# Kernel optimization log

Measured on AMD Instinct MI355X. Metric: run time of the kernel, lower is better.

## Reference

```python
import jax, jax.numpy as jnp
import numpy as np

STRIDE, PAD, DIL = 1, 1, 1
EPS = 1e-12
RHO_LIM = 1.0 - 1e-6
PI = jnp.pi


def clamp_pg(x, lo=0.0):
    # clamp value but pass gradient through (clamp_preserve_grad)
    return x + jax.lax.stop_gradient(jnp.maximum(x, lo) - x)


def setup_inputs() -> dict:
    key = jax.random.key(0)
    B, N, T, K = 8, 128, 1024, 3
    k = jax.random.uniform(key, (B, B, N, T, 2), dtype=jnp.float32)
    leak = jnp.array(1.0, dtype=jnp.float32)
    alpha = jnp.full((1, 1, K), 1.0 / K, dtype=jnp.float32)
    beta = jnp.array(0.0, dtype=jnp.float32)
    return {"k": k, "leak": leak, "alpha": alpha, "beta": beta}


def reference(k, leak, alpha, beta):
    k_gp, k_ntk = k[..., 0], k[..., 1]          # (B,B,N,T) each
    B, _, N, T = k_gp.shape

    # v[b,t] = k_gp[b,b,0,t]  (diagonal over batch dims, first lag)
    ar = jnp.arange(B)
    v = k_gp[ar, ar, 0, :]                      # (B,T)
    v_pad = jnp.pad(v, ((0, 0), (0, N - 1)))    # (B, T+N-1)

    v_xx = v[:, None, None, :]                  # (B,1,1,T)
    idx = jnp.arange(N)[:, None] + jnp.arange(T)[None, :]  # (N,T)
    v_yy = v_pad[:, idx][None]                  # (1,B,N,T): v_pad[b, n+t]

    # calculate_statistics
    std_x = jnp.sqrt(jnp.maximum(v_xx, 0.0))
    std_y = jnp.sqrt(jnp.maximum(v_yy, 0.0))
    denom = jnp.maximum(std_x * std_y, EPS)
    rho = jnp.clip(k_gp / denom, -RHO_LIM, RHO_LIM)  # (B,B,N,T)

    a = clamp_pg(leak)
    theta = jnp.arccos(rho)
    s = jnp.sqrt(1.0 - rho * rho)
    one_m = (1.0 - a) ** 2
    coef = 1.0 + a * a
    # leaky-ReLU arccos kernel and its derivative kernel
    c0 = std_x * std_y / (2.0 * PI) * (one_m * s + rho * (coef * PI - one_m * theta))
    c1 = (coef * PI - one_m * theta) / (2.0 * PI)

    w = clamp_pg(alpha)                         # (1,1,K)

    def conv(x):  # x: (B,B,N,T) -> (B,B,N,T')
        y = jax.lax.conv_general_dilated(
            x.reshape(-1, 1, T), w, window_strides=(STRIDE,),
            padding=[(PAD, PAD)], rhs_dilation=(DIL,),
            dimension_numbers=("NCH", "OIH", "NCH"))
        return y.reshape(B, B, N, -1)

    kg = conv(c0)
    kn = conv(c1 * k_ntk) + kg

    b = clamp_pg(beta)
    kg = kg + b
    kn = kn + b
    return jnp.stack([kg, kn], axis=-1)
```

## Files before the change

### kernel.cpp

```cpp
#include <hip/hip_runtime.h>
#include <math.h>

#define BDIM 8
#define NDIM 128
#define TDIM 1024
#define TPB 512
#define ROWS 4
#define LSTRIDE 1028

#define EPS_F 1e-12f
#define RHO_LIM_F (1.0f - 1e-6f)
#define PI_F 3.14159265358979323846f


__device__ __forceinline__ void kfun(float kgp, float kntk, float vx, float vy,
                                     float one_m, float coef, bool fast,
                                     float& c0, float& cn)
{
    const float inv2pi = 0.15915494309189535f;
    const float p = sqrtf(fmaxf(vx, 0.0f) * fmaxf(vy, 0.0f));
    if (fast) {
        const float hc = 0.5f * coef;
        const float pr = p * RHO_LIM_F;
        c0 = hc * fminf(fmaxf(kgp, -pr), pr);
        cn = hc * kntk;
    } else {
        const float r  = fminf(fmaxf(kgp * __builtin_amdgcn_rcpf(fmaxf(p, EPS_F)), -RHO_LIM_F), RHO_LIM_F);
        const float th = acosf(r);
        const float s  = sqrtf(1.0f - r * r);
        const float br = coef * PI_F - one_m * th;
        c0 = p * inv2pi * (one_m * s + r * br);
        cn = br * inv2pi * kntk;
    }
}

__global__ __launch_bounds__(TPB) void conv_arccos_kernel(
    const float* __restrict__ k,
    const float* __restrict__ leak,
    const float* __restrict__ alpha,
    const float* __restrict__ beta,
    float* __restrict__ out)
{
    __shared__ float sc0[ROWS * LSTRIDE];
    __shared__ float scn[ROWS * LSTRIDE];

    const int base = blockIdx.x * ROWS;
    const int n0   = base % NDIM;
    const int bb   = base / NDIM;
    const int b2   = bb % BDIM;
    const int b1   = bb / BDIM;
    const int tid  = threadIdx.x;
    const int t    = tid * 2;

    const float a   = fmaxf(leak[0], 0.0f);
    const float w0  = fmaxf(alpha[0], 0.0f);
    const float w1  = fmaxf(alpha[1], 0.0f);
    const float w2  = fmaxf(alpha[2], 0.0f);
    const float bia = fmaxf(beta[0], 0.0f);

    const float one_m = (1.0f - a) * (1.0f - a);
    const float coef  = 1.0f + a * a;
    const bool  fast  = (one_m == 0.0f);

    const float2* vrx = (const float2*)(k) + (size_t)(b1 * BDIM + b1) * NDIM * TDIM;
    const float2* vry = (const float2*)(k) + (size_t)(b2 * BDIM + b2) * NDIM * TDIM;

    if (tid < ROWS * 2) {
        const int r   = tid >> 1;
        const int idx = r * LSTRIDE + ((tid & 1) ? (TDIM + 1) : 0);
        sc0[idx] = 0.0f;
        scn[idx] = 0.0f;
    }

    const float4 vx2 = ((const float4*)vrx)[tid];
    const float4* vyp = (const float4*)(vry + (n0 + t));
    const float4 vyA = vyp[0];
    const float4 vyB = vyp[1];
    float y0 = vyA.x, y1 = vyA.z, y2 = vyB.x, y3 = vyB.z;
    float y4 = vry[n0 + t + 4].x;
    const int ty = n0 + t;
    if (ty     >= TDIM) y0 = 0.0f;
    if (ty + 1 >= TDIM) y1 = 0.0f;
    if (ty + 2 >= TDIM) y2 = 0.0f;
    if (ty + 3 >= TDIM) y3 = 0.0f;
    if (ty + 4 >= TDIM) y4 = 0.0f;
    const float yv[6] = { y0, y1, y2, y3, y4, 0.0f };

    #pragma unroll
    for (int rl = 0; rl < ROWS; ++rl) {
        const float4 kv = ((const float4*)(k + (size_t)(base + rl) * TDIM * 2))[tid];
        float c00, cn0, c01, cn1;
        kfun(kv.x, kv.y, vx2.x, yv[rl],     one_m, coef, fast, c00, cn0);
        kfun(kv.z, kv.w, vx2.z, yv[rl + 1], one_m, coef, fast, c01, cn1);
        const int bi = rl * LSTRIDE + t + 1;
        sc0[bi]     = c00;
        sc0[bi + 1] = c01;
        scn[bi]     = cn0;
        scn[bi + 1] = cn1;
    }

    __syncthreads();

    #pragma unroll
    for (int rl = 0; rl < ROWS; ++rl) {
        const int bi = rl * LSTRIDE + t;
        const float c0l = sc0[bi], c00 = sc0[bi + 1], c01 = sc0[bi + 2], c0r = sc0[bi + 3];
        const float cnl = scn[bi], cn0 = scn[bi + 1], cn1 = scn[bi + 2], cnr = scn[bi + 3];

        const float kg0 = fmaf(w0, c0l, fmaf(w1, c00, fmaf(w2, c01, bia)));
        const float kg1 = fmaf(w0, c00, fmaf(w1, c01, fmaf(w2, c0r, bia)));
        const float kn0 = fmaf(w0, cnl, fmaf(w1, cn0, fmaf(w2, cn1, kg0)));
        const float kn1 = fmaf(w0, cn0, fmaf(w1, cn1, fmaf(w2, cnr, kg1)));

        float4 o;
        o.x = kg0; o.y = kn0; o.z = kg1; o.w = kn1;
        ((float4*)(out + (size_t)(base + rl) * TDIM * 2))[tid] = o;
    }
}

extern "C" void kernel_launch(void* const* d_in, const int* in_sizes, int n_in,
                              void* d_out, int out_size, void* d_ws, size_t ws_size,
                              hipStream_t stream) {
    const float* k     = (const float*)d_in[0];
    const float* leak  = (const float*)d_in[1];
    const float* alpha = (const float*)d_in[2];
    const float* beta  = (const float*)d_in[3];
    float* out = (float*)d_out;

    const int n_blocks = BDIM * BDIM * NDIM / ROWS;
    conv_arccos_kernel<<<n_blocks, TPB, 0, stream>>>(k, leak, alpha, beta, out);
}
```

Before: 118.5 us.

## Map one wavefront per row and exchange conv halos via shuffles

```diff
diff --git a/kernel.cpp b/kernel.cpp
--- a/kernel.cpp
+++ b/kernel.cpp
@@ -5,20 +5,20 @@
 #define NDIM 128
 #define TDIM 1024
 #define TPB 512
-#define ROWS 4
-#define LSTRIDE 1028
+#define ROWS_PER_BLOCK 8
 
 #define EPS_F 1e-12f
 #define RHO_LIM_F (1.0f - 1e-6f)
 #define PI_F 3.14159265358979323846f
 
+typedef float nfloat4 __attribute__((ext_vector_type(4)));
 
-__device__ __forceinline__ void kfun(float kgp, float kntk, float vx, float vy,
-                                     float one_m, float coef, bool fast,
-                                     float& c0, float& cn)
+__device__ __forceinline__ void kfun2(float kgp, float kntk, float sx, float sy,
+                                      float one_m, float coef, bool fast,
+                                      float& c0, float& cn)
 {
     const float inv2pi = 0.15915494309189535f;
-    const float p = sqrtf(fmaxf(vx, 0.0f) * fmaxf(vy, 0.0f));
+    const float p = sx * sy;
     if (fast) {
         const float hc = 0.5f * coef;
         const float pr = p * RHO_LIM_F;
@@ -41,16 +41,13 @@
     const float* __restrict__ beta,
     float* __restrict__ out)
 {
-    __shared__ float sc0[ROWS * LSTRIDE];
-    __shared__ float scn[ROWS * LSTRIDE];
-
-    const int base = blockIdx.x * ROWS;
-    const int n0   = base % NDIM;
-    const int bb   = base / NDIM;
-    const int b2   = bb % BDIM;
-    const int b1   = bb / BDIM;
-    const int tid  = threadIdx.x;
-    const int t    = tid * 2;
+    const int wid  = threadIdx.x >> 6;
+    const int lane = threadIdx.x & 63;
+    const int row  = blockIdx.x * ROWS_PER_BLOCK + wid;
+    const int n    = row & (NDIM - 1);
+    const int bb   = row >> 7;
+    const int b2   = bb & (BDIM - 1);
+    const int b1   = bb >> 3;
 
     const float a   = fmaxf(leak[0], 0.0f);
     const float w0  = fmaxf(alpha[0], 0.0f);
@@ -62,59 +59,59 @@
     const float coef  = 1.0f + a * a;
     const bool  fast  = (one_m == 0.0f);
 
-    const float2* vrx = (const float2*)(k) + (size_t)(b1 * BDIM + b1) * NDIM * TDIM;
-    const float2* vry = (const float2*)(k) + (size_t)(b2 * BDIM + b2) * NDIM * TDIM;
+    const nfloat4* krow = (const nfloat4*)(k + (size_t)row * TDIM * 2);
+    nfloat4*       orow = (nfloat4*)(out + (size_t)row * TDIM * 2);
+    const float2* vrx = (const float2*)k + (size_t)(b1 * BDIM + b1) * NDIM * TDIM;
+    const float2* vry = (const float2*)k + (size_t)(b2 * BDIM + b2) * NDIM * TDIM;
 
-    if (tid < ROWS * 2) {
-        const int r   = tid >> 1;
-        const int idx = r * LSTRIDE + ((tid & 1) ? (TDIM + 1) : 0);
-        sc0[idx] = 0.0f;
-        scn[idx] = 0.0f;
-    }
+    auto compute = [&](int m, float& c00, float& c01, float& cn0, float& cn1) {
+        const int p  = (m << 6) + lane;
+        const int t0 = p * 2;
+        const nfloat4 kv = __builtin_nontemporal_load(&krow[p]);
+        const float4 vx4 = *(const float4*)(vrx + t0);
+        const int e = n + t0;
+        const float2 vya = vry[e];
+        const float2 vyb = vry[e + 1];
+        const float y0 = (e     < TDIM) ? vya.x : 0.0f;
+        const float y1 = (e + 1 < TDIM) ? vyb.x : 0.0f;
+        const float sx0 = sqrtf(fmaxf(vx4.x, 0.0f));
+        const float sx1 = sqrtf(fmaxf(vx4.z, 0.0f));
+        const float sy0 = sqrtf(fmaxf(y0, 0.0f));
+        const float sy1 = sqrtf(fmaxf(y1, 0.0f));
+        kfun2(kv.x, kv.y, sx0, sy0, one_m, coef, fast, c00, cn0);
+        kfun2(kv.z, kv.w, sx1, sy1, one_m, coef, fast, c01, cn1);
+    };
 
-    const float4 vx2 = ((const float4*)vrx)[tid];
-    const float4* vyp = (const float4*)(vry + (n0 + t));
-    const float4 vyA = vyp[0];
-    const float4 vyB = vyp[1];
-    float y0 = vyA.x, y1 = vyA.z, y2 = vyB.x, y3 = vyB.z;
-    float y4 = vry[n0 + t + 4].x;
-    const int ty = n0 + t;
-    if (ty     >= TDIM) y0 = 0.0f;
-    if (ty + 1 >= TDIM) y1 = 0.0f;
-    if (ty + 2 >= TDIM) y2 = 0.0f;
-    if (ty + 3 >= TDIM) y3 = 0.0f;
-    if (ty + 4 >= TDIM) y4 = 0.0f;
-    const float yv[6] = { y0, y1, y2, y3, y4, 0.0f };
+    float c00, c01, cn0, cn1;
+    compute(0, c00, c01, cn0, cn1);
+    float pe0 = 0.0f, pen = 0.0f;
 
     #pragma unroll
-    for (int rl = 0; rl < ROWS; ++rl) {
-        const float4 kv = ((const float4*)(k + (size_t)(base + rl) * TDIM * 2))[tid];
-        float c00, cn0, c01, cn1;
-        kfun(kv.x, kv.y, vx2.x, yv[rl],     one_m, coef, fast, c00, cn0);
-        kfun(kv.z, kv.w, vx2.z, yv[rl + 1], one_m, coef, fast, c01, cn1);
-        const int bi = rl * LSTRIDE + t + 1;
-        sc0[bi]     = c00;
-        sc0[bi + 1] = c01;
-        scn[bi]     = cn0;
-        scn[bi + 1] = cn1;
-    }
+    for (int m = 0; m < 8; ++m) {
+        float n00 = 0.0f, n01 = 0.0f, nn0 = 0.0f, nn1 = 0.0f;
+        if (m < 7) compute(m + 1, n00, n01, nn0, nn1);
+        const float nx0 = __shfl(n00, 0);
+        const float nxn = __shfl(nn0, 0);
 
-    __syncthreads();
-
-    #pragma unroll
-    for (int rl = 0; rl < ROWS; ++rl) {
-        const int bi = rl * LSTRIDE + t;
-        const float c0l = sc0[bi], c00 = sc0[bi + 1], c01 = sc0[bi + 2], c0r = sc0[bi + 3];
-        const float cnl = scn[bi], cn0 = scn[bi + 1], cn1 = scn[bi + 2], cnr = scn[bi + 3];
+        float c0l = __shfl_up(c01, 1);
+        float cnl = __shfl_up(cn1, 1);
+        if (lane == 0) { c0l = pe0; cnl = pen; }
+        float c0r = __shfl_down(c00, 1);
+        float cnr = __shfl_down(cn0, 1);
+        if (lane == 63) { c0r = nx0; cnr = nxn; }
 
         const float kg0 = fmaf(w0, c0l, fmaf(w1, c00, fmaf(w2, c01, bia)));
         const float kg1 = fmaf(w0, c00, fmaf(w1, c01, fmaf(w2, c0r, bia)));
         const float kn0 = fmaf(w0, cnl, fmaf(w1, cn0, fmaf(w2, cn1, kg0)));
         const float kn1 = fmaf(w0, cn0, fmaf(w1, cn1, fmaf(w2, cnr, kg1)));
 
-        float4 o;
+        nfloat4 o;
         o.x = kg0; o.y = kn0; o.z = kg1; o.w = kn1;
-        ((float4*)(out + (size_t)(base + rl) * TDIM * 2))[tid] = o;
+        __builtin_nontemporal_store(o, &orow[(m << 6) + lane]);
+
+        pe0 = __shfl(c01, 63);
+        pen = __shfl(cn1, 63);
+        c00 = n00; c01 = n01; cn0 = nn0; cn1 = nn1;
     }
 }
 
@@ -127,6 +124,6 @@
     const float* beta  = (const float*)d_in[3];
     float* out = (float*)d_out;
 
-    const int n_blocks = BDIM * BDIM * NDIM / ROWS;
+    const int n_blocks = BDIM * BDIM * NDIM / ROWS_PER_BLOCK;
     conv_arccos_kernel<<<n_blocks, TPB, 0, stream>>>(k, leak, alpha, beta, out);
 }
```

New measurement: 129.9 us. 1.1x slower.

## Replace shared-memory halo exchange with redundant neighbor loads and recompute

Applied to the files above, without the earlier changes.

```diff
diff --git a/kernel.cpp b/kernel.cpp
--- a/kernel.cpp
+++ b/kernel.cpp
@@ -6,19 +6,17 @@
 #define TDIM 1024
 #define TPB 512
 #define ROWS 4
-#define LSTRIDE 1028
 
 #define EPS_F 1e-12f
 #define RHO_LIM_F (1.0f - 1e-6f)
 #define PI_F 3.14159265358979323846f
 
-
-__device__ __forceinline__ void kfun(float kgp, float kntk, float vx, float vy,
+__device__ __forceinline__ void kfun(float kgp, float kntk, float sx, float sy,
                                      float one_m, float coef, bool fast,
                                      float& c0, float& cn)
 {
     const float inv2pi = 0.15915494309189535f;
-    const float p = sqrtf(fmaxf(vx, 0.0f) * fmaxf(vy, 0.0f));
+    const float p = sx * sy;
     if (fast) {
         const float hc = 0.5f * coef;
         const float pr = p * RHO_LIM_F;
@@ -41,9 +39,6 @@
     const float* __restrict__ beta,
     float* __restrict__ out)
 {
-    __shared__ float sc0[ROWS * LSTRIDE];
-    __shared__ float scn[ROWS * LSTRIDE];
-
     const int base = blockIdx.x * ROWS;
     const int n0   = base % NDIM;
     const int bb   = base / NDIM;
@@ -65,47 +60,47 @@
     const float2* vrx = (const float2*)(k) + (size_t)(b1 * BDIM + b1) * NDIM * TDIM;
     const float2* vry = (const float2*)(k) + (size_t)(b2 * BDIM + b2) * NDIM * TDIM;
 
-    if (tid < ROWS * 2) {
-        const int r   = tid >> 1;
-        const int idx = r * LSTRIDE + ((tid & 1) ? (TDIM + 1) : 0);
-        sc0[idx] = 0.0f;
-        scn[idx] = 0.0f;
+    const float4 vx4 = ((const float4*)vrx)[tid];
+    const float vxm  = vrx[max(t - 1, 0)].x;
+    const float vxp  = vrx[min(t + 2, TDIM - 1)].x;
+    const float sxm  = (tid == 0)       ? 0.0f : sqrtf(fmaxf(vxm, 0.0f));
+    const float sx0  = sqrtf(fmaxf(vx4.x, 0.0f));
+    const float sx1  = sqrtf(fmaxf(vx4.z, 0.0f));
+    const float sxp  = (tid == TPB - 1) ? 0.0f : sqrtf(fmaxf(vxp, 0.0f));
+
+    const int e0 = n0 + t;
+    const float4 vyA = *(const float4*)(vry + e0);
+    const float4 vyB = *(const float4*)(vry + e0 + 2);
+    const float4 vyC = *(const float4*)(vry + e0 + 4);
+    const float  ym  = vry[max(e0 - 1, 0)].x;
+
+    float sy[7];
+    {
+        const float yv[7] = { ym, vyA.x, vyA.z, vyB.x, vyB.z, vyC.x, vyC.z };
+        #pragma unroll
+        for (int j = 0; j < 7; ++j) {
+            const int e = e0 - 1 + j;
+            const float y = (e >= 0 && e < TDIM) ? yv[j] : 0.0f;
+            sy[j] = sqrtf(fmaxf(y, 0.0f));
+        }
     }
-
-    const float4 vx2 = ((const float4*)vrx)[tid];
-    const float4* vyp = (const float4*)(vry + (n0 + t));
-    const float4 vyA = vyp[0];
-    const float4 vyB = vyp[1];
-    float y0 = vyA.x, y1 = vyA.z, y2 = vyB.x, y3 = vyB.z;
-    float y4 = vry[n0 + t + 4].x;
-    const int ty = n0 + t;
-    if (ty     >= TDIM) y0 = 0.0f;
-    if (ty + 1 >= TDIM) y1 = 0.0f;
-    if (ty + 2 >= TDIM) y2 = 0.0f;
-    if (ty + 3 >= TDIM) y3 = 0.0f;
-    if (ty + 4 >= TDIM) y4 = 0.0f;
-    const float yv[6] = { y0, y1, y2, y3, y4, 0.0f };
 
     #pragma unroll
     for (int rl = 0; rl < ROWS; ++rl) {
-        const float4 kv = ((const float4*)(k + (size_t)(base + rl) * TDIM * 2))[tid];
-        float c00, cn0, c01, cn1;
-        kfun(kv.x, kv.y, vx2.x, yv[rl],     one_m, coef, fast, c00, cn0);
-        kfun(kv.z, kv.w, vx2.z, yv[rl + 1], one_m, coef, fast, c01, cn1);
-        const int bi = rl * LSTRIDE + t + 1;
-        sc0[bi]     = c00;
-        sc0[bi + 1] = c01;
-        scn[bi]     = cn0;
-        scn[bi + 1] = cn1;
-    }
+        const float* krow = k + (size_t)(base + rl) * TDIM * 2;
+        const float4 kv = ((const float4*)krow)[tid];
+        const float2 kl = ((const float2*)krow)[max(t - 1, 0)];
+        const float2 kr = ((const float2*)krow)[min(t + 2, TDIM - 1)];
+        const float klg = (tid == 0)       ? 0.0f : kl.x;
+        const float kln = (tid == 0)       ? 0.0f : kl.y;
+        const float krg = (tid == TPB - 1) ? 0.0f : kr.x;
+        const float krn = (tid == TPB - 1) ? 0.0f : kr.y;
 
-    __syncthreads();
-
-    #pragma unroll
-    for (int rl = 0; rl < ROWS; ++rl) {
-        const int bi = rl * LSTRIDE + t;
-        const float c0l = sc0[bi], c00 = sc0[bi + 1], c01 = sc0[bi + 2], c0r = sc0[bi + 3];
-        const float cnl = scn[bi], cn0 = scn[bi + 1], cn1 = scn[bi + 2], cnr = scn[bi + 3];
+        float c0l, cnl, c00, cn0, c01, cn1, c0r, cnr;
+        kfun(klg,  kln,  sxm, sy[rl + 0], one_m, coef, fast, c0l, cnl);
+        kfun(kv.x, kv.y, sx0, sy[rl + 1], one_m, coef, fast, c00, cn0);
+        kfun(kv.z, kv.w, sx1, sy[rl + 2], one_m, coef, fast, c01, cn1);
+        kfun(krg,  krn,  sxp, sy[rl + 3], one_m, coef, fast, c0r, cnr);
 
         const float kg0 = fmaf(w0, c0l, fmaf(w1, c00, fmaf(w2, c01, bia)));
         const float kg1 = fmaf(w0, c00, fmaf(w1, c01, fmaf(w2, c0r, bia)));
```

Result: slower. 129.5 us (+9.3%).
